# Performance work log

Hardware: AMD Instinct MI355X
Metric: run time of the kernel (lower is better)

Reference implementation:

```python
import jax, jax.numpy as jnp
import numpy as np

PLACEHOLDER = -1
TINY = np.float32(np.finfo(np.float32).tiny)

B, S, V = 128, 8, 32000  # batch, max_spec_len, vocab


def setup_inputs() -> dict:
    key = jax.random.key(0)
    ks = jax.random.split(key, 8)
    # probability tables from softmaxed logits (faithful: rows sum to 1)
    draft_probs = jax.nn.softmax(2.0 * jax.random.normal(ks[0], (B, S, V), dtype=jnp.float32), axis=-1)
    target_probs = jax.nn.softmax(2.0 * jax.random.normal(ks[1], (B, S + 1, V), dtype=jnp.float32), axis=-1)
    draft_token_ids = jax.random.randint(ks[2], (B, S), 0, V, dtype=jnp.int64)
    # variable number of draft tokens per sequence; tail padded with PLACEHOLDER
    lens = jax.random.randint(ks[3], (B,), 1, S + 1)
    draft_token_ids = jnp.where(jnp.arange(S)[None, :] < lens[:, None], draft_token_ids, PLACEHOLDER)
    bonus_token_ids = jax.random.randint(ks[4], (B,), 0, V, dtype=jnp.int64)
    uniform_probs = jax.random.uniform(ks[5], (B, S), dtype=jnp.float32, minval=1e-6, maxval=1.0)
    exp_q = jax.random.exponential(ks[6], (B, V), dtype=jnp.float32)  # q.exponential_()
    is_greedy = jax.random.bernoulli(ks[7], 0.3, (B,))  # temperature == -1 per sequence
    return {
        "draft_token_ids": draft_token_ids,
        "draft_probs": draft_probs,
        "target_probs": target_probs,
        "bonus_token_ids": bonus_token_ids,
        "uniform_probs": uniform_probs,
        "exp_q": exp_q,
        "is_greedy": is_greedy,
    }


def reference(draft_token_ids, draft_probs, target_probs, bonus_token_ids,
              uniform_probs, exp_q, is_greedy):
    b, s = draft_token_ids.shape
    valid = draft_token_ids != PLACEHOLDER                      # [B,S]
    safe_tok = jnp.where(valid, draft_token_ids, 0)

    # gather p_target(tok), p_draft(tok) at each speculative position
    tp = jnp.take_along_axis(target_probs[:, :s], safe_tok[..., None], axis=2)[..., 0]
    dp = jnp.take_along_axis(draft_probs, safe_tok[..., None], axis=2)[..., 0]
    random_accept = (tp / dp) >= uniform_probs                  # [B,S]

    target_argmax = jnp.argmax(target_probs, axis=-1)           # [B,S+1]
    greedy_accept = draft_token_ids == target_argmax[:, :s]

    accept = jnp.where(is_greedy[:, None], greedy_accept, random_accept)

    # recovered token on rejection: argmax of normalized clamp(target - draft) / Exp noise
    adjusted = jnp.clip(target_probs[:, :s] - draft_probs, TINY, None)
    adjusted = adjusted / jnp.sum(adjusted, axis=-1, keepdims=True)
    recovered = jnp.argmax(adjusted / exp_q[:, None, :], axis=-1)  # [B,S]
    replacement = jnp.where(is_greedy[:, None], target_argmax[:, :s], recovered)

    # sequential early-exit scan, vectorized: position p emits iff all earlier
    # positions were valid & accepted and p itself is valid
    step = (valid & accept).astype(jnp.int32)
    alive_prefix = jnp.concatenate(
        [jnp.ones((b, 1), jnp.int32), jnp.cumprod(step, axis=1)[:, :-1]], axis=1).astype(bool)
    emit = valid & alive_prefix                                 # [B,S]

    tokens = jnp.where(accept, draft_token_ids, replacement)
    out = jnp.full((b, s + 1), PLACEHOLDER, dtype=jnp.int64)
    out = out.at[:, :s].set(jnp.where(emit, tokens, PLACEHOLDER))

    num_generated = jnp.sum(emit, axis=1)                       # [B]
    rejected = jnp.any(emit & ~accept, axis=1)                  # [B]
    bonus_val = jnp.where(rejected, PLACEHOLDER, bonus_token_ids)
    out = out.at[jnp.arange(b), num_generated].set(bonus_val)
    return out
```

## Files before the change

kernel.cpp:

```cpp
#include <hip/hip_runtime.h>

#define PLACEHOLDER (-1)
#define TINY_F 1.17549435e-38f
#define MAXS 32
#define SPLIT_G 8
#define SPLIT_R 16

__device__ __forceinline__ void amax_combine(float& bv, int& bi, float v, int i) {
    if (v > bv || (v == bv && i < bi)) { bv = v; bi = i; }
}

__device__ __forceinline__ unsigned long long pack_vi(float v, int i) {
    return ((unsigned long long)__float_as_uint(v) << 32) |
           (unsigned long long)(0xFFFFFFFFu - (unsigned)i);
}

__device__ __forceinline__ int unpack_idx(unsigned long long p) {
    return (int)(0xFFFFFFFFu - (unsigned)(p & 0xFFFFFFFFull));
}

__device__ __forceinline__ void block_argmax(float& bv, int& bi) {
    for (int off = 32; off > 0; off >>= 1) {
        float ov = __shfl_down(bv, off, 64);
        int   oi = __shfl_down(bi, off, 64);
        amax_combine(bv, bi, ov, oi);
    }
    __shared__ float sv[8];
    __shared__ int   si[8];
    int lane = threadIdx.x & 63;
    int w    = threadIdx.x >> 6;
    if (lane == 0) { sv[w] = bv; si[w] = bi; }
    __syncthreads();
    if (threadIdx.x == 0) {
        int nw = (blockDim.x + 63) >> 6;
        for (int k = 1; k < nw; ++k) amax_combine(bv, bi, sv[k], si[k]);
    }
}

__global__ void k_main(const float* __restrict__ target_probs,
                       const float* __restrict__ draft_probs,
                       const float* __restrict__ exp_q,
                       const int* __restrict__ draft_ids,
                       const float* __restrict__ uniform,
                       const int* __restrict__ is_greedy,
                       unsigned long long* __restrict__ ws_g,
                       unsigned long long* __restrict__ ws_r,
                       int B, int S, int V) {
    int total_g = B * SPLIT_G;

    if ((int)blockIdx.x < total_g) {
        int b = blockIdx.x / SPLIT_G;
        int split = blockIdx.x - b * SPLIT_G;
        if (!is_greedy[b]) return;
        if (draft_ids[b * S] == PLACEHOLDER) return;

        int chunk = ((V + SPLIT_G - 1) / SPLIT_G + 3) & ~3;
        int begin = split * chunk;
        int end = begin + chunk; if (end > V) end = V;
        if (begin >= end) return;

        const float* row = target_probs + (size_t)b * (S + 1) * V;
        float bv = 0.0f; int bi = 0x7fffffff;
        int vend = begin + ((end - begin) & ~3);
        const float4* r4 = (const float4*)row;
        for (int j = (begin >> 2) + threadIdx.x; j < (vend >> 2); j += blockDim.x) {
            float4 f = r4[j];
            int base = j << 2;
            amax_combine(bv, bi, f.x, base);
            amax_combine(bv, bi, f.y, base + 1);
            amax_combine(bv, bi, f.z, base + 2);
            amax_combine(bv, bi, f.w, base + 3);
        }
        for (int j = vend + threadIdx.x; j < end; j += blockDim.x)
            amax_combine(bv, bi, row[j], j);
        block_argmax(bv, bi);
        if (threadIdx.x == 0) ws_g[(size_t)b * SPLIT_G + split] = pack_vi(bv, bi);
    } else {
        int t = blockIdx.x - total_g;
        int split = t % SPLIT_R;
        int b = t / SPLIT_R;
        if (is_greedy[b]) return;

        __shared__ int s_tok[MAXS];
        __shared__ unsigned char s_acc[MAXS];
        __shared__ int s_fr;
        int p = threadIdx.x;
        if (p < S) {
            int tok = draft_ids[b * S + p];
            s_tok[p] = tok;
            bool acc = false;
            if (tok != PLACEHOLDER) {
                float tp = target_probs[(size_t)b * (S + 1) * V + (size_t)p * V + tok];
                float dp = draft_probs[(size_t)b * S * V + (size_t)p * V + tok];
                acc = (tp / dp) >= uniform[b * S + p];
            }
            s_acc[p] = acc ? 1 : 0;
        }
        __syncthreads();
        if (threadIdx.x == 0) {
            int fr = -1;
            for (int q = 0; q < S; ++q) {
                if (s_tok[q] == PLACEHOLDER) break;
                if (!s_acc[q]) { fr = q; break; }
            }
            s_fr = fr;
        }
        __syncthreads();
        int fr = s_fr;
        if (fr < 0) return;

        int chunk = ((V + SPLIT_R - 1) / SPLIT_R + 3) & ~3;
        int begin = split * chunk;
        int end = begin + chunk; if (end > V) end = V;
        if (begin >= end) return;

        const float* trow = target_probs + (size_t)b * (S + 1) * V + (size_t)fr * V;
        const float* drow = draft_probs + (size_t)b * S * V + (size_t)fr * V;
        const float* erow = exp_q + (size_t)b * V;
        float bv = 0.0f; int bi = 0x7fffffff;
        int vend = begin + ((end - begin) & ~3);
        const float4* t4 = (const float4*)trow;
        const float4* d4 = (const float4*)drow;
        const float4* e4 = (const float4*)erow;
        for (int j = (begin >> 2) + threadIdx.x; j < (vend >> 2); j += blockDim.x) {
            float4 tt = t4[j], dd = d4[j], ee = e4[j];
            int base = j << 2;
            amax_combine(bv, bi, fmaxf(tt.x - dd.x, TINY_F) / ee.x, base);
            amax_combine(bv, bi, fmaxf(tt.y - dd.y, TINY_F) / ee.y, base + 1);
            amax_combine(bv, bi, fmaxf(tt.z - dd.z, TINY_F) / ee.z, base + 2);
            amax_combine(bv, bi, fmaxf(tt.w - dd.w, TINY_F) / ee.w, base + 3);
        }
        for (int j = vend + threadIdx.x; j < end; j += blockDim.x)
            amax_combine(bv, bi, fmaxf(trow[j] - drow[j], TINY_F) / erow[j], j);
        block_argmax(bv, bi);
        if (threadIdx.x == 0) ws_r[(size_t)b * SPLIT_R + split] = pack_vi(bv, bi);
    }
}

__global__ void k_final(const int* __restrict__ draft_ids,
                        const float* __restrict__ draft_probs,
                        const float* __restrict__ target_probs,
                        const int* __restrict__ bonus,
                        const float* __restrict__ uniform,
                        const int* __restrict__ is_greedy,
                        const unsigned long long* __restrict__ ws_g,
                        const unsigned long long* __restrict__ ws_r,
                        int* __restrict__ out,
                        int B, int S, int V) {
    int b = blockIdx.x;
    int tid = threadIdx.x;
    bool greedy = is_greedy[b] != 0;
    int ob = b * (S + 1);

    __shared__ int s_am;

    if (greedy) {
        int p = 0, ng = 0;
        bool rej = false;
        while (p < S) {
            int tok = draft_ids[b * S + p];
            if (tok == PLACEHOLDER) break;
            __syncthreads();
            if (p == 0) {
                if (tid == 0) {
                    unsigned long long m = 0ull;
                    const unsigned long long* g = ws_g + (size_t)b * SPLIT_G;
                    int chunk = ((V + SPLIT_G - 1) / SPLIT_G + 3) & ~3;
                    for (int k = 0; k < SPLIT_G; ++k)
                        if (k * chunk < V) { unsigned long long x = g[k]; if (x > m) m = x; }
                    s_am = unpack_idx(m);
                }
            } else {
                const float* row = target_probs + (size_t)b * (S + 1) * V + (size_t)p * V;
                float bv = 0.0f; int bi = 0x7fffffff;
                int nv4 = V >> 2;
                const float4* r4 = (const float4*)row;
                for (int j = tid; j < nv4; j += blockDim.x) {
                    float4 f = r4[j];
                    int base = j << 2;
                    amax_combine(bv, bi, f.x, base);
                    amax_combine(bv, bi, f.y, base + 1);
                    amax_combine(bv, bi, f.z, base + 2);
                    amax_combine(bv, bi, f.w, base + 3);
                }
                for (int j = (nv4 << 2) + tid; j < V; j += blockDim.x)
                    amax_combine(bv, bi, row[j], j);
                block_argmax(bv, bi);
                if (tid == 0) s_am = bi;
            }
            __syncthreads();
            int am = s_am;
            bool acc = (tok == am);
            if (tid == 0) out[ob + p] = acc ? tok : am;
            ++ng;
            if (!acc) { rej = true; break; }
            ++p;
        }
        if (tid == 0) {
            for (int q = ng; q <= S; ++q) out[ob + q] = PLACEHOLDER;
            if (!rej) out[ob + ng] = bonus[b];
        }
    } else {
        __shared__ int s_tok[MAXS];
        __shared__ unsigned char s_acc[MAXS];
        if (tid < S) {
            int tok = draft_ids[b * S + tid];
            s_tok[tid] = tok;
            bool acc = false;
            if (tok != PLACEHOLDER) {
                float tp = target_probs[(size_t)b * (S + 1) * V + (size_t)tid * V + tok];
                float dp = draft_probs[(size_t)b * S * V + (size_t)tid * V + tok];
                acc = (tp / dp) >= uniform[b * S + tid];
            }
            s_acc[tid] = acc ? 1 : 0;
        }
        __syncthreads();
        if (tid == 0) {
            unsigned long long rm = 0ull;
            const unsigned long long* r = ws_r + (size_t)b * SPLIT_R;
            int chunk = ((V + SPLIT_R - 1) / SPLIT_R + 3) & ~3;

            int ng = 0;
            bool rej = false;
            for (int p = 0; p < S; ++p) {
                int tok = s_tok[p];
                if (tok == PLACEHOLDER) break;
                bool acc = s_acc[p] != 0;
                if (acc) {
                    out[ob + p] = tok;
                    ++ng;
                } else {
                    for (int k = 0; k < SPLIT_R; ++k)
                        if (k * chunk < V) { unsigned long long x = r[k]; if (x > rm) rm = x; }
                    out[ob + p] = unpack_idx(rm);
                    ++ng;
                    rej = true;
                    break;
                }
            }
            for (int q = ng; q <= S; ++q) out[ob + q] = PLACEHOLDER;
            if (!rej) out[ob + ng] = bonus[b];
        }
    }
}

extern "C" void kernel_launch(void* const* d_in, const int* in_sizes, int n_in,
                              void* d_out, int out_size, void* d_ws, size_t ws_size,
                              hipStream_t stream) {
    const int*   draft_ids    = (const int*)d_in[0];
    const float* draft_probs  = (const float*)d_in[1];
    const float* target_probs = (const float*)d_in[2];
    const int*   bonus        = (const int*)d_in[3];
    const float* uniform      = (const float*)d_in[4];
    const float* exp_q        = (const float*)d_in[5];
    const int*   is_greedy    = (const int*)d_in[6];

    int B = in_sizes[6];
    int S = in_sizes[4] / B;
    int V = in_sizes[5] / B;

    unsigned long long* ws_g = (unsigned long long*)d_ws;
    unsigned long long* ws_r = ws_g + (size_t)B * SPLIT_G;
    int* out = (int*)d_out;

    int grid = B * SPLIT_G + B * SPLIT_R;
    k_main<<<grid, 256, 0, stream>>>(target_probs, draft_probs, exp_q, draft_ids,
                                     uniform, is_greedy, ws_g, ws_r, B, S, V);
    k_final<<<B, 256, 0, stream>>>(draft_ids, draft_probs, target_probs, bonus,
                                   uniform, is_greedy, ws_g, ws_r, out, B, S, V);
}
```

Before: 16.30 us.

## Prefetch exp noise before accept scan and move output writes into main kernel

The random-sampling blocks now issue their exp_q chunk loads before the acceptance scan, so that memory latency overlaps the dependent gather and first-rejection search. Accepted-prefix output writes are moved into k_main, and the first-rejection position is stored in workspace, leaving k_final with only a small reduction of per-split results. k_final drops to a single 64-thread wave with shuffle-based reductions and no barriers. The greedy path for positions after the first now scans a full vocab row with one wave instead of four, which can lengthen that serial tail.

```diff
diff --git a/kernel.cpp b/kernel.cpp
--- a/kernel.cpp
+++ b/kernel.cpp
@@ -37,14 +37,27 @@
     }
 }
 
+__device__ __forceinline__ void wave_argmax_bcast(float& bv, int& bi) {
+    for (int off = 32; off > 0; off >>= 1) {
+        float ov = __shfl_down(bv, off, 64);
+        int   oi = __shfl_down(bi, off, 64);
+        amax_combine(bv, bi, ov, oi);
+    }
+    bv = __shfl(bv, 0, 64);
+    bi = __shfl(bi, 0, 64);
+}
+
 __global__ void k_main(const float* __restrict__ target_probs,
                        const float* __restrict__ draft_probs,
                        const float* __restrict__ exp_q,
                        const int* __restrict__ draft_ids,
                        const float* __restrict__ uniform,
+                       const int* __restrict__ bonus,
                        const int* __restrict__ is_greedy,
                        unsigned long long* __restrict__ ws_g,
                        unsigned long long* __restrict__ ws_r,
+                       int* __restrict__ ws_fr,
+                       int* __restrict__ out,
                        int B, int S, int V) {
     int total_g = B * SPLIT_G;
 
@@ -81,128 +94,22 @@
         int b = t / SPLIT_R;
         if (is_greedy[b]) return;
 
+        int chunk = ((V + SPLIT_R - 1) / SPLIT_R + 3) & ~3;
+        int begin = split * chunk;
+        int end = begin + chunk; if (end > V) end = V;
+        bool has_work = begin < end;
+
+        const float* erow = exp_q + (size_t)b * V;
+        int nj = has_work ? (((end - begin) & ~3) >> 2) : 0;
+        const float4* e4 = (const float4*)(erow + begin);
+        int tid = threadIdx.x;
+        float4 ea = make_float4(0.f, 0.f, 0.f, 0.f), eb = ea;
+        if (tid < nj) ea = e4[tid];
+        if (tid + (int)blockDim.x < nj) eb = e4[tid + blockDim.x];
+
         __shared__ int s_tok[MAXS];
         __shared__ unsigned char s_acc[MAXS];
         __shared__ int s_fr;
-        int p = threadIdx.x;
-        if (p < S) {
-            int tok = draft_ids[b * S + p];
-            s_tok[p] = tok;
-            bool acc = false;
-            if (tok != PLACEHOLDER) {
-                float tp = target_probs[(size_t)b * (S + 1) * V + (size_t)p * V + tok];
-                float dp = draft_probs[(size_t)b * S * V + (size_t)p * V + tok];
-                acc = (tp / dp) >= uniform[b * S + p];
-            }
-            s_acc[p] = acc ? 1 : 0;
-        }
-        __syncthreads();
-        if (threadIdx.x == 0) {
-            int fr = -1;
-            for (int q = 0; q < S; ++q) {
-                if (s_tok[q] == PLACEHOLDER) break;
-                if (!s_acc[q]) { fr = q; break; }
-            }
-            s_fr = fr;
-        }
-        __syncthreads();
-        int fr = s_fr;
-        if (fr < 0) return;
-
-        int chunk = ((V + SPLIT_R - 1) / SPLIT_R + 3) & ~3;
-        int begin = split * chunk;
-        int end = begin + chunk; if (end > V) end = V;
-        if (begin >= end) return;
-
-        const float* trow = target_probs + (size_t)b * (S + 1) * V + (size_t)fr * V;
-        const float* drow = draft_probs + (size_t)b * S * V + (size_t)fr * V;
-        const float* erow = exp_q + (size_t)b * V;
-        float bv = 0.0f; int bi = 0x7fffffff;
-        int vend = begin + ((end - begin) & ~3);
-        const float4* t4 = (const float4*)trow;
-        const float4* d4 = (const float4*)drow;
-        const float4* e4 = (const float4*)erow;
-        for (int j = (begin >> 2) + threadIdx.x; j < (vend >> 2); j += blockDim.x) {
-            float4 tt = t4[j], dd = d4[j], ee = e4[j];
-            int base = j << 2;
-            amax_combine(bv, bi, fmaxf(tt.x - dd.x, TINY_F) / ee.x, base);
-            amax_combine(bv, bi, fmaxf(tt.y - dd.y, TINY_F) / ee.y, base + 1);
-            amax_combine(bv, bi, fmaxf(tt.z - dd.z, TINY_F) / ee.z, base + 2);
-            amax_combine(bv, bi, fmaxf(tt.w - dd.w, TINY_F) / ee.w, base + 3);
-        }
-        for (int j = vend + threadIdx.x; j < end; j += blockDim.x)
-            amax_combine(bv, bi, fmaxf(trow[j] - drow[j], TINY_F) / erow[j], j);
-        block_argmax(bv, bi);
-        if (threadIdx.x == 0) ws_r[(size_t)b * SPLIT_R + split] = pack_vi(bv, bi);
-    }
-}
-
-__global__ void k_final(const int* __restrict__ draft_ids,
-                        const float* __restrict__ draft_probs,
-                        const float* __restrict__ target_probs,
-                        const int* __restrict__ bonus,
-                        const float* __restrict__ uniform,
-                        const int* __restrict__ is_greedy,
-                        const unsigned long long* __restrict__ ws_g,
-                        const unsigned long long* __restrict__ ws_r,
-                        int* __restrict__ out,
-                        int B, int S, int V) {
-    int b = blockIdx.x;
-    int tid = threadIdx.x;
-    bool greedy = is_greedy[b] != 0;
-    int ob = b * (S + 1);
-
-    __shared__ int s_am;
-
-    if (greedy) {
-        int p = 0, ng = 0;
-        bool rej = false;
-        while (p < S) {
-            int tok = draft_ids[b * S + p];
-            if (tok == PLACEHOLDER) break;
-            __syncthreads();
-            if (p == 0) {
-                if (tid == 0) {
-                    unsigned long long m = 0ull;
-                    const unsigned long long* g = ws_g + (size_t)b * SPLIT_G;
-                    int chunk = ((V + SPLIT_G - 1) / SPLIT_G + 3) & ~3;
-                    for (int k = 0; k < SPLIT_G; ++k)
-                        if (k * chunk < V) { unsigned long long x = g[k]; if (x > m) m = x; }
-                    s_am = unpack_idx(m);
-                }
-            } else {
-                const float* row = target_probs + (size_t)b * (S + 1) * V + (size_t)p * V;
-                float bv = 0.0f; int bi = 0x7fffffff;
-                int nv4 = V >> 2;
-                const float4* r4 = (const float4*)row;
-                for (int j = tid; j < nv4; j += blockDim.x) {
-                    float4 f = r4[j];
-                    int base = j << 2;
-                    amax_combine(bv, bi, f.x, base);
-                    amax_combine(bv, bi, f.y, base + 1);
-                    amax_combine(bv, bi, f.z, base + 2);
-                    amax_combine(bv, bi, f.w, base + 3);
-                }
-                for (int j = (nv4 << 2) + tid; j < V; j += blockDim.x)
-                    amax_combine(bv, bi, row[j], j);
-                block_argmax(bv, bi);
-                if (tid == 0) s_am = bi;
-            }
-            __syncthreads();
-            int am = s_am;
-            bool acc = (tok == am);
-            if (tid == 0) out[ob + p] = acc ? tok : am;
-            ++ng;
-            if (!acc) { rej = true; break; }
-            ++p;
-        }
-        if (tid == 0) {
-            for (int q = ng; q <= S; ++q) out[ob + q] = PLACEHOLDER;
-            if (!rej) out[ob + ng] = bonus[b];
-        }
-    } else {
-        __shared__ int s_tok[MAXS];
-        __shared__ unsigned char s_acc[MAXS];
         if (tid < S) {
             int tok = draft_ids[b * S + tid];
             s_tok[tid] = tok;
@@ -216,31 +123,149 @@
         }
         __syncthreads();
         if (tid == 0) {
-            unsigned long long rm = 0ull;
-            const unsigned long long* r = ws_r + (size_t)b * SPLIT_R;
-            int chunk = ((V + SPLIT_R - 1) / SPLIT_R + 3) & ~3;
-
-            int ng = 0;
-            bool rej = false;
-            for (int p = 0; p < S; ++p) {
-                int tok = s_tok[p];
-                if (tok == PLACEHOLDER) break;
-                bool acc = s_acc[p] != 0;
-                if (acc) {
-                    out[ob + p] = tok;
+            int fr = -1;
+            for (int q = 0; q < S; ++q) {
+                if (s_tok[q] == PLACEHOLDER) break;
+                if (!s_acc[q]) { fr = q; break; }
+            }
+            s_fr = fr;
+        }
+        __syncthreads();
+        int fr = s_fr;
+
+        if (split == 0 && tid == 0) {
+            ws_fr[b] = fr;
+            int ob = b * (S + 1);
+            if (fr < 0) {
+                int ng = 0;
+                for (int p = 0; p < S; ++p) {
+                    if (s_tok[p] == PLACEHOLDER) break;
+                    out[ob + p] = s_tok[p];
                     ++ng;
-                } else {
-                    for (int k = 0; k < SPLIT_R; ++k)
-                        if (k * chunk < V) { unsigned long long x = r[k]; if (x > rm) rm = x; }
-                    out[ob + p] = unpack_idx(rm);
-                    ++ng;
-                    rej = true;
-                    break;
                 }
-            }
+                for (int q = ng; q <= S; ++q) out[ob + q] = PLACEHOLDER;
+                out[ob + ng] = bonus[b];
+            } else {
+                for (int p = 0; p < fr; ++p) out[ob + p] = s_tok[p];
+                for (int q = fr; q <= S; ++q) out[ob + q] = PLACEHOLDER;
+            }
+        }
+        if (fr < 0 || !has_work) return;
+
+        const float* trow = target_probs + (size_t)b * (S + 1) * V + (size_t)fr * V;
+        const float* drow = draft_probs + (size_t)b * S * V + (size_t)fr * V;
+        const float4* t4 = (const float4*)(trow + begin);
+        const float4* d4 = (const float4*)(drow + begin);
+        float bv = 0.0f; int bi = 0x7fffffff;
+        if (tid < nj) {
+            float4 tt = t4[tid], dd = d4[tid];
+            int base = begin + (tid << 2);
+            amax_combine(bv, bi, fmaxf(tt.x - dd.x, TINY_F) / ea.x, base);
+            amax_combine(bv, bi, fmaxf(tt.y - dd.y, TINY_F) / ea.y, base + 1);
+            amax_combine(bv, bi, fmaxf(tt.z - dd.z, TINY_F) / ea.z, base + 2);
+            amax_combine(bv, bi, fmaxf(tt.w - dd.w, TINY_F) / ea.w, base + 3);
+        }
+        if (tid + (int)blockDim.x < nj) {
+            int j = tid + blockDim.x;
+            float4 tt = t4[j], dd = d4[j];
+            int base = begin + (j << 2);
+            amax_combine(bv, bi, fmaxf(tt.x - dd.x, TINY_F) / eb.x, base);
+            amax_combine(bv, bi, fmaxf(tt.y - dd.y, TINY_F) / eb.y, base + 1);
+            amax_combine(bv, bi, fmaxf(tt.z - dd.z, TINY_F) / eb.z, base + 2);
+            amax_combine(bv, bi, fmaxf(tt.w - dd.w, TINY_F) / eb.w, base + 3);
+        }
+        for (int j = tid + 2 * blockDim.x; j < nj; j += blockDim.x) {
+            float4 tt = t4[j], dd = d4[j], ee = e4[j];
+            int base = begin + (j << 2);
+            amax_combine(bv, bi, fmaxf(tt.x - dd.x, TINY_F) / ee.x, base);
+            amax_combine(bv, bi, fmaxf(tt.y - dd.y, TINY_F) / ee.y, base + 1);
+            amax_combine(bv, bi, fmaxf(tt.z - dd.z, TINY_F) / ee.z, base + 2);
+            amax_combine(bv, bi, fmaxf(tt.w - dd.w, TINY_F) / ee.w, base + 3);
+        }
+        for (int j = begin + (nj << 2) + tid; j < end; j += blockDim.x)
+            amax_combine(bv, bi, fmaxf(trow[j] - drow[j], TINY_F) / erow[j], j);
+        block_argmax(bv, bi);
+        if (tid == 0) ws_r[(size_t)b * SPLIT_R + split] = pack_vi(bv, bi);
+    }
+}
+
+__global__ void k_final(const int* __restrict__ draft_ids,
+                        const float* __restrict__ target_probs,
+                        const int* __restrict__ bonus,
+                        const int* __restrict__ is_greedy,
+                        const unsigned long long* __restrict__ ws_g,
+                        const unsigned long long* __restrict__ ws_r,
+                        const int* __restrict__ ws_fr,
+                        int* __restrict__ out,
+                        int B, int S, int V) {
+    int b = blockIdx.x;
+    int lane = threadIdx.x;
+    int ob = b * (S + 1);
+
+    if (is_greedy[b]) {
+        unsigned long long gm = 0ull;
+        {
+            int chunk = ((V + SPLIT_G - 1) / SPLIT_G + 3) & ~3;
+            if (lane < SPLIT_G && lane * chunk < V)
+                gm = ws_g[(size_t)b * SPLIT_G + lane];
+        }
+        for (int off = SPLIT_G / 2; off > 0; off >>= 1) {
+            unsigned long long o = __shfl_down(gm, off, 64);
+            if (o > gm) gm = o;
+        }
+        gm = __shfl(gm, 0, 64);
+        int am0 = unpack_idx(gm);
+
+        int p = 0, ng = 0;
+        bool rej = false;
+        while (p < S) {
+            int tok = draft_ids[b * S + p];
+            if (tok == PLACEHOLDER) break;
+            int am;
+            if (p == 0) {
+                am = am0;
+            } else {
+                const float* row = target_probs + (size_t)b * (S + 1) * V + (size_t)p * V;
+                float bv = 0.0f; int bi = 0x7fffffff;
+                int nv4 = V >> 2;
+                const float4* r4 = (const float4*)row;
+                for (int j = lane; j < nv4; j += 64) {
+                    float4 f = r4[j];
+                    int base = j << 2;
+                    amax_combine(bv, bi, f.x, base);
+                    amax_combine(bv, bi, f.y, base + 1);
+                    amax_combine(bv, bi, f.z, base + 2);
+                    amax_combine(bv, bi, f.w, base + 3);
+                }
+                for (int j = (nv4 << 2) + lane; j < V; j += 64)
+                    amax_combine(bv, bi, row[j], j);
+                wave_argmax_bcast(bv, bi);
+                am = bi;
+            }
+            bool acc = (tok == am);
+            if (lane == 0) out[ob + p] = acc ? tok : am;
+            ++ng;
+            if (!acc) { rej = true; break; }
+            ++p;
+        }
+        if (lane == 0) {
             for (int q = ng; q <= S; ++q) out[ob + q] = PLACEHOLDER;
             if (!rej) out[ob + ng] = bonus[b];
         }
+    } else {
+        int fr = ws_fr[b];
+        if (fr < 0) return;
+        unsigned long long rm = 0ull;
+        {
+            int chunk = ((V + SPLIT_R - 1) / SPLIT_R + 3) & ~3;
+            if (lane < SPLIT_R && lane * chunk < V)
+                rm = ws_r[(size_t)b * SPLIT_R + lane];
+        }
+        for (int off = SPLIT_R / 2; off > 0; off >>= 1) {
+            unsigned long long o = __shfl_down(rm, off, 64);
+            if (o > rm) rm = o;
+        }
+        if (lane == 0) out[ob + fr] = unpack_idx(rm);
     }
 }
 
@@ -261,11 +286,13 @@
 
     unsigned long long* ws_g = (unsigned long long*)d_ws;
     unsigned long long* ws_r = ws_g + (size_t)B * SPLIT_G;
+    int* ws_fr = (int*)(ws_r + (size_t)B * SPLIT_R);
     int* out = (int*)d_out;
 
     int grid = B * SPLIT_G + B * SPLIT_R;
     k_main<<<grid, 256, 0, stream>>>(target_probs, draft_probs, exp_q, draft_ids,
-                                     uniform, is_greedy, ws_g, ws_r, B, S, V);
-    k_final<<<B, 256, 0, stream>>>(draft_ids, draft_probs, target_probs, bonus,
-                                   uniform, is_greedy, ws_g, ws_r, out, B, S, V);
-}
+                                     uniform, bonus, is_greedy,
+                                     ws_g, ws_r, ws_fr, out, B, S, V);
+    k_final<<<B, 64, 0, stream>>>(draft_ids, target_probs, bonus, is_greedy,
+                                  ws_g, ws_r, ws_fr, out, B, S, V);
+}
```

After: 15.21 us. 6.7% less time.
